# Kernel optimization log

Measured on AMD Instinct MI355X. Metric: run time of the kernel, lower is better.

The kernel has to match this reference:

```python
import jax, jax.numpy as jnp
import numpy as np

N_NODES = 100000
N_EDGES = 3200000
NFEAT = 512
NHID = 256
KEEP_PROB = 0.5  # dropout p = 0.5


def setup_inputs() -> dict:
    key = jax.random.key(0)
    ks = jax.random.split(key, 9)
    x = jax.random.normal(ks[0], (N_NODES, NFEAT), dtype=jnp.float32)
    W1 = jax.random.normal(ks[1], (NFEAT, NHID), dtype=jnp.float32) * (1.0 / np.sqrt(NFEAT))
    b1 = jax.random.normal(ks[2], (NHID,), dtype=jnp.float32) * 0.01
    W2 = jax.random.normal(ks[3], (NHID, NHID), dtype=jnp.float32) * (1.0 / np.sqrt(NHID))
    b2 = jax.random.normal(ks[4], (NHID,), dtype=jnp.float32) * 0.01
    edge_row = jnp.sort(jax.random.randint(ks[5], (N_EDGES,), 0, N_NODES, dtype=jnp.int64))
    edge_col = jax.random.randint(ks[6], (N_EDGES,), 0, N_NODES, dtype=jnp.int64)
    edge_weight = jax.random.uniform(ks[7], (N_EDGES,), dtype=jnp.float32)
    drop_u = jax.random.uniform(ks[8], (N_NODES, NHID), dtype=jnp.float32)
    return {"x": x, "W1": W1, "b1": b1, "W2": W2, "b2": b2,
            "edge_row": edge_row, "edge_col": edge_col,
            "edge_weight": edge_weight, "drop_u": drop_u}


def reference(x, W1, b1, W2, b2, edge_row, edge_col, edge_weight, drop_u):
    n = x.shape[0]

    def spmm(h):
        # out[i] = sum_j adj[i, j] * h[j]  (COO gather + segment-sum)
        msg = h[edge_col] * edge_weight[:, None]  # [E, d]
        return jax.ops.segment_sum(msg, edge_row, num_segments=n)

    # layer 1: relu(spmm(adj, x @ W1) + b1)
    h = jax.nn.relu(spmm(x @ W1) + b1)
    # deterministic dropout (training=True, p=0.5): keep where u < keep_prob, scale by 1/keep
    mask = (drop_u < KEEP_PROB).astype(h.dtype)
    h = h * mask / KEEP_PROB
    # layer 2: relu(spmm(adj, h @ W2) + b2)
    h = jax.nn.relu(spmm(h @ W2) + b2)
    return jax.nn.log_softmax(h, axis=1)
```

## Files before the change

### kernel.cpp

```cpp
#include <hip/hip_runtime.h>
#include <stdint.h>

#define N_NODES 100000
#define N_EDGES 3200000
#define NFEAT 512
#define NHID 256
#define MPAD 100096

typedef __attribute__((ext_vector_type(8))) short bf16x8_t;
typedef __attribute__((ext_vector_type(8))) unsigned short u16x8_t;
typedef __attribute__((ext_vector_type(4))) float f32x4_t;

#define RFL(x) __builtin_amdgcn_readfirstlane(x)

__device__ inline unsigned short f2bf(float f) {
  union { float f; uint32_t u; } x; x.f = f;
  uint32_t r = x.u + 0x7fffu + ((x.u >> 16) & 1u);
  return (unsigned short)(r >> 16);
}
__device__ inline float b2f(unsigned short u) {
  union { uint32_t u; float f; } x; x.u = ((uint32_t)u) << 16;
  return x.f;
}

__global__ void prep_k(const float* __restrict__ W1, const float* __restrict__ W2,
                       unsigned short* __restrict__ W1T, unsigned short* __restrict__ W2T) {
  int i = blockIdx.x * 256 + threadIdx.x;
  if (i < NFEAT * NHID) {
    int k = i >> 8, n = i & 255;
    W1T[n * NFEAT + k] = f2bf(W1[i]);
  } else {
    int j = i - NFEAT * NHID;
    int k = j >> 8, n = j & 255;
    W2T[n * NHID + k] = f2bf(W2[j]);
  }
}

__global__ void rowptr_k(const int* __restrict__ erow, int* __restrict__ rowptr) {
  int r = blockIdx.x * 256 + threadIdx.x;
  if (r > N_NODES) return;
  int lo = 0, hi = N_EDGES;
  while (lo < hi) {
    int mid = (lo + hi) >> 1;
    if (erow[mid] < r) lo = mid + 1; else hi = mid;
  }
  rowptr[r] = lo;
}

template <bool A_FP32>
__global__ __launch_bounds__(512) void gemm_bt2(const void* __restrict__ Ap,
                                                const unsigned short* __restrict__ BT,
                                                unsigned short* __restrict__ C,
                                                int K, int Mreal) {
  __shared__ __align__(16) unsigned short As[128 * 64];
  __shared__ __align__(16) unsigned short Bs[256 * 64];
  const int tid = threadIdx.x;
  const int lane = tid & 63, wid = tid >> 6;
  const int wm = wid >> 2, wn = wid & 3;
  const int m0 = blockIdx.x * 128;
  const int lrow = lane & 15, lhi = lane >> 4;

  f32x4_t acc[4][4] = {};

  const int nt = K >> 6;
  for (int t = 0; t < nt; ++t) {
    __syncthreads();
    if constexpr (A_FP32) {
      const float* A = (const float*)Ap;
      const int rr = tid >> 4;
      const int kq = (tid & 15) << 2;
#pragma unroll
      for (int round = 0; round < 4; ++round) {
        int row = rr + (round << 5);
        int grow = m0 + row; grow = grow < Mreal ? grow : Mreal - 1;
        const f32x4_t v = __builtin_nontemporal_load(
            (const f32x4_t*)(A + (size_t)grow * K + (t << 6) + kq));
        ushort4 b4;
        b4.x = f2bf(v.x); b4.y = f2bf(v.y); b4.z = f2bf(v.z); b4.w = f2bf(v.w);
        *(ushort4*)&As[(row << 6) + (kq ^ ((row & 7) << 3))] = b4;
      }
    } else {
      const unsigned short* A = (const unsigned short*)Ap;
      const int Lrow = tid >> 3;
      const int Lc = (tid & 7) << 4;
#pragma unroll
      for (int round = 0; round < 2; ++round) {
        int row = Lrow + (round << 6);
        int srcc = Lc ^ ((row & 7) << 4);
        const char* g = (const char*)(A + (size_t)(m0 + row) * K + (t << 6)) + srcc;
        __builtin_amdgcn_global_load_lds(
            (const __attribute__((address_space(1))) void*)g,
            (__attribute__((address_space(3))) void*)((char*)As + tid * 16 + (round << 13)),
            16, 0, 0);
      }
    }
    {
      const int Lrow = tid >> 3;
      const int Lc = (tid & 7) << 4;
#pragma unroll
      for (int round = 0; round < 4; ++round) {
        int row = Lrow + (round << 6);
        int srcc = Lc ^ ((row & 7) << 4);
        const char* g = (const char*)(BT + (size_t)row * K + (t << 6)) + srcc;
        __builtin_amdgcn_global_load_lds(
            (const __attribute__((address_space(1))) void*)g,
            (__attribute__((address_space(3))) void*)((char*)Bs + tid * 16 + (round << 13)),
            16, 0, 0);
      }
    }
    asm volatile("s_waitcnt vmcnt(0)" ::: "memory");
    __syncthreads();

#pragma unroll
    for (int ks = 0; ks < 2; ++ks) {
      bf16x8_t af[4], bfr[4];
      const int cu = (ks << 5) + (lhi << 3);
#pragma unroll
      for (int mf = 0; mf < 4; ++mf) {
        int row = (wm << 6) + (mf << 4) + lrow;
        af[mf] = *(const bf16x8_t*)&As[(row << 6) + (cu ^ ((row & 7) << 3))];
      }
#pragma unroll
      for (int nf = 0; nf < 4; ++nf) {
        int row = (wn << 6) + (nf << 4) + lrow;
        bfr[nf] = *(const bf16x8_t*)&Bs[(row << 6) + (cu ^ ((row & 7) << 3))];
      }
#pragma unroll
      for (int mf = 0; mf < 4; ++mf)
#pragma unroll
        for (int nf = 0; nf < 4; ++nf)
          acc[mf][nf] = __builtin_amdgcn_mfma_f32_16x16x32_bf16(af[mf], bfr[nf], acc[mf][nf], 0, 0, 0);
    }
  }

#pragma unroll
  for (int mf = 0; mf < 4; ++mf)
#pragma unroll
    for (int nf = 0; nf < 4; ++nf)
#pragma unroll
      for (int j = 0; j < 4; ++j) {
        int gm = m0 + (wm << 6) + (mf << 4) + (lhi << 2) + j;
        int gn = (wn << 6) + (nf << 4) + lrow;
        C[(size_t)gm * 256 + gn] = f2bf(acc[mf][nf][j]);
      }
}

#define LOADP4(V, W, EB)                                             \
  _Pragma("unroll")                                                  \
  for (int q = 0; q < 4; ++q) {                                      \
    uint32_t ce = (uint32_t)RFL(ecol[(EB) + 2 * q]);                 \
    uint32_t co = (uint32_t)RFL(ecol[(EB) + 2 * q + 1]);             \
    uint32_t ue = RFL(__float_as_uint(ew[(EB) + 2 * q]));            \
    uint32_t uo = RFL(__float_as_uint(ew[(EB) + 2 * q + 1]));        \
    uint32_t cv = lo ? ce : co;                                      \
    W[q] = __uint_as_float(lo ? ue : uo);                            \
    V[q] = *(const u16x8_t*)(Xb + (((size_t)cv << 9) + c16));        \
  }
#define CONSP4(V, W)                                                 \
  _Pragma("unroll")                                                  \
  for (int q = 0; q < 4; ++q)                                        \
    _Pragma("unroll")                                                \
    for (int j = 0; j < 8; ++j)                                      \
      f[j] += W[q] * b2f(V[q][j]);

#define GATHER_ROW()                                                 \
  u16x8_t va[4], vb[4]; float wa[4], wb[4];                          \
  if (e + 8 <= e1) {                                                 \
    LOADP4(va, wa, e);                                               \
    for (; e + 24 <= e1; e += 16) {                                  \
      LOADP4(vb, wb, e + 8);                                         \
      CONSP4(va, wa);                                                \
      LOADP4(va, wa, e + 16);                                        \
      CONSP4(vb, wb);                                                \
    }                                                                \
    if (e + 16 <= e1) {                                              \
      LOADP4(vb, wb, e + 8);                                         \
      CONSP4(va, wa);                                                \
      CONSP4(vb, wb);                                                \
      e += 16;                                                       \
    } else { CONSP4(va, wa); e += 8; }                               \
  }                                                                  \
  for (; e < e1; ++e) {         \
    uint32_t c = (uint32_t)RFL(ecol[e]);                             \
    float w = __uint_as_float(RFL(__float_as_uint(ew[e])));          \
    u16x8_t v = *(const u16x8_t*)(Xb + (((size_t)c << 9) + c16));    \
    float wv = lo ? w : 0.0f;                                        \
    _Pragma("unroll")                                                \
    for (int j = 0; j < 8; ++j) f[j] += wv * b2f(v[j]);              \
  }                                                                  \
  _Pragma("unroll")                                                  \
  for (int j = 0; j < 8; ++j) f[j] += __shfl_xor(f[j], 32);

__global__ __launch_bounds__(256) void spmm1_k(const unsigned short* __restrict__ XW1,
                                               const int* __restrict__ rowptr,
                                               const int* __restrict__ ecol,
                                               const float* __restrict__ ew,
                                               const float* __restrict__ b1,
                                               const float* __restrict__ du,
                                               unsigned short* __restrict__ H) {
  const int lane = threadIdx.x & 63, wid = threadIdx.x >> 6;
  const int r = blockIdx.x * 4 + wid;
  const bool lo = lane < 32;
  const int g = lane & 31;
  const uint32_t c16 = (uint32_t)g << 4;
  if (r >= N_NODES) {
    if (lo) {
      u16x8_t z;
#pragma unroll
      for (int j = 0; j < 8; ++j) z[j] = 0;
      *(u16x8_t*)&H[(size_t)r * 256 + (g << 3)] = z;
    }
    return;
  }
  const char* Xb = (const char*)XW1;
  float f[8] = {};
  int e  = RFL(rowptr[r]);
  const int e1 = RFL(rowptr[r + 1]);
  GATHER_ROW();
  if (lo) {
    const int g8 = g << 3;
    float bv[8], uu[8];
    *(f32x4_t*)&bv[0] = *(const f32x4_t*)&b1[g8];
    *(f32x4_t*)&bv[4] = *(const f32x4_t*)&b1[g8 + 4];
    *(f32x4_t*)&uu[0] = __builtin_nontemporal_load((const f32x4_t*)&du[(size_t)r * 256 + g8]);
    *(f32x4_t*)&uu[4] = __builtin_nontemporal_load((const f32x4_t*)&du[(size_t)r * 256 + g8 + 4]);
    u16x8_t o;
#pragma unroll
    for (int j = 0; j < 8; ++j) {
      float h = fmaxf(f[j] + bv[j], 0.f) * (uu[j] < 0.5f ? 2.f : 0.f);
      o[j] = f2bf(h);
    }
    *(u16x8_t*)&H[(size_t)r * 256 + g8] = o;
  }
}

__global__ __launch_bounds__(256) void spmm2_k(const unsigned short* __restrict__ HW2,
                                               const int* __restrict__ rowptr,
                                               const int* __restrict__ ecol,
                                               const float* __restrict__ ew,
                                               const float* __restrict__ b2,
                                               float* __restrict__ out) {
  const int lane = threadIdx.x & 63, wid = threadIdx.x >> 6;
  const int r = blockIdx.x * 4 + wid;
  if (r >= N_NODES) return;
  const bool lo = lane < 32;
  const int g = lane & 31;
  const uint32_t c16 = (uint32_t)g << 4;
  const char* Xb = (const char*)HW2;
  float f[8] = {};
  int e  = RFL(rowptr[r]);
  const int e1 = RFL(rowptr[r + 1]);
  GATHER_ROW();
  const int g8 = g << 3;
  float bv[8];
  *(f32x4_t*)&bv[0] = *(const f32x4_t*)&b2[g8];
  *(f32x4_t*)&bv[4] = *(const f32x4_t*)&b2[g8 + 4];
  float v[8];
#pragma unroll
  for (int j = 0; j < 8; ++j) v[j] = fmaxf(f[j] + bv[j], 0.f);
  float m = v[0];
#pragma unroll
  for (int j = 1; j < 8; ++j) m = fmaxf(m, v[j]);
#pragma unroll
  for (int off = 16; off > 0; off >>= 1) m = fmaxf(m, __shfl_xor(m, off));
  float s = 0.f;
#pragma unroll
  for (int j = 0; j < 8; ++j) s += expf(v[j] - m);
#pragma unroll
  for (int off = 16; off > 0; off >>= 1) s += __shfl_xor(s, off);
  const float ls = m + logf(s);
  if (lo) {
    f32x4_t o0, o1;
    o0.x = v[0] - ls; o0.y = v[1] - ls; o0.z = v[2] - ls; o0.w = v[3] - ls;
    o1.x = v[4] - ls; o1.y = v[5] - ls; o1.z = v[6] - ls; o1.w = v[7] - ls;
    __builtin_nontemporal_store(o0, (f32x4_t*)&out[(size_t)r * 256 + g8]);
    __builtin_nontemporal_store(o1, (f32x4_t*)&out[(size_t)r * 256 + g8 + 4]);
  }
}

extern "C" void kernel_launch(void* const* d_in, const int* in_sizes, int n_in,
                              void* d_out, int out_size, void* d_ws, size_t ws_size,
                              hipStream_t stream) {
  const float* x  = (const float*)d_in[0];
  const float* W1 = (const float*)d_in[1];
  const float* b1 = (const float*)d_in[2];
  const float* W2 = (const float*)d_in[3];
  const float* b2 = (const float*)d_in[4];
  const int* erow = (const int*)d_in[5];
  const int* ecol = (const int*)d_in[6];
  const float* ew = (const float*)d_in[7];
  const float* du = (const float*)d_in[8];
  float* out = (float*)d_out;

  char* ws = (char*)d_ws;
  unsigned short* W1T = (unsigned short*)ws;
  unsigned short* W2T = (unsigned short*)(ws + 262144);
  int* rowptr = (int*)(ws + 262144 + 131072);
  unsigned short* XW1 = (unsigned short*)(ws + 262144 + 131072 + 401408);
  unsigned short* H = (unsigned short*)(ws + 262144 + 131072 + 401408 + 51249152);

  prep_k<<<768, 256, 0, stream>>>(W1, W2, W1T, W2T);
  rowptr_k<<<392, 256, 0, stream>>>(erow, rowptr);
  gemm_bt2<true><<<782, 512, 0, stream>>>((const void*)x, W1T, XW1, NFEAT, N_NODES);
  spmm1_k<<<MPAD / 4, 256, 0, stream>>>(XW1, rowptr, ecol, ew, b1, du, H);
  gemm_bt2<false><<<782, 512, 0, stream>>>((const void*)H, W2T, XW1, NHID, MPAD);
  spmm2_k<<<N_NODES / 4, 256, 0, stream>>>(XW1, rowptr, ecol, ew, b2, out);
}
```

Measured before the change: 547.6 us.

## Split SpMM gathers into two column-half passes to shrink gather working set

Measured after the change: 547.9 us. Within noise of the previous version (+0.0%).

```diff
diff --git a/kernel.cpp b/kernel.cpp
--- a/kernel.cpp
+++ b/kernel.cpp
@@ -8,7 +8,7 @@
 #define MPAD 100096
 
 typedef __attribute__((ext_vector_type(8))) short bf16x8_t;
-typedef __attribute__((ext_vector_type(8))) unsigned short u16x8_t;
+typedef __attribute__((ext_vector_type(4))) unsigned short u16x4_t;
 typedef __attribute__((ext_vector_type(4))) float f32x4_t;
 
 #define RFL(x) __builtin_amdgcn_readfirstlane(x)
@@ -154,17 +154,17 @@
     uint32_t uo = RFL(__float_as_uint(ew[(EB) + 2 * q + 1]));        \
     uint32_t cv = lo ? ce : co;                                      \
     W[q] = __uint_as_float(lo ? ue : uo);                            \
-    V[q] = *(const u16x8_t*)(Xb + (((size_t)cv << 9) + c16));        \
+    V[q] = *(const u16x4_t*)(Xb + (((size_t)cv << 9) + c8));         \
   }
 #define CONSP4(V, W)                                                 \
   _Pragma("unroll")                                                  \
   for (int q = 0; q < 4; ++q)                                        \
     _Pragma("unroll")                                                \
-    for (int j = 0; j < 8; ++j)                                      \
+    for (int j = 0; j < 4; ++j)                                      \
       f[j] += W[q] * b2f(V[q][j]);
 
 #define GATHER_ROW()                                                 \
-  u16x8_t va[4], vb[4]; float wa[4], wb[4];                          \
+  u16x4_t va[4], vb[4]; float wa[4], wb[4];                          \
   if (e + 8 <= e1) {                                                 \
     LOADP4(va, wa, e);                                               \
     for (; e + 24 <= e1; e += 16) {                                  \
@@ -181,17 +181,18 @@
     } else { CONSP4(va, wa); e += 8; }                               \
   }                                                                  \
   for (; e < e1; ++e) {         \
-    uint32_t c = (uint32_t)RFL(ecol[e]);                             \
-    float w = __uint_as_float(RFL(__float_as_uint(ew[e])));          \
-    u16x8_t v = *(const u16x8_t*)(Xb + (((size_t)c << 9) + c16));    \
-    float wv = lo ? w : 0.0f;                                        \
+    uint32_t c_ = (uint32_t)RFL(ecol[e]);                            \
+    float w_ = __uint_as_float(RFL(__float_as_uint(ew[e])));         \
+    u16x4_t v_ = *(const u16x4_t*)(Xb + (((size_t)c_ << 9) + c8));   \
+    float wv_ = lo ? w_ : 0.0f;                                      \
     _Pragma("unroll")                                                \
-    for (int j = 0; j < 8; ++j) f[j] += wv * b2f(v[j]);              \
+    for (int j = 0; j < 4; ++j) f[j] += wv_ * b2f(v_[j]);            \
   }                                                                  \
   _Pragma("unroll")                                                  \
-  for (int j = 0; j < 8; ++j) f[j] += __shfl_xor(f[j], 32);
-
-__global__ __launch_bounds__(256) void spmm1_k(const unsigned short* __restrict__ XW1,
+  for (int j = 0; j < 4; ++j) f[j] += __shfl_xor(f[j], 32);
+
+template <int P>
+__global__ __launch_bounds__(256) void spmm1_h(const unsigned short* __restrict__ XW1,
                                                const int* __restrict__ rowptr,
                                                const int* __restrict__ ecol,
                                                const float* __restrict__ ew,
@@ -202,80 +203,99 @@
   const int r = blockIdx.x * 4 + wid;
   const bool lo = lane < 32;
   const int g = lane & 31;
-  const uint32_t c16 = (uint32_t)g << 4;
+  const uint32_t c8 = (uint32_t)g << 3;
+  const int g4 = g << 2;
   if (r >= N_NODES) {
     if (lo) {
-      u16x8_t z;
-#pragma unroll
-      for (int j = 0; j < 8; ++j) z[j] = 0;
-      *(u16x8_t*)&H[(size_t)r * 256 + (g << 3)] = z;
+      ushort4 z; z.x = z.y = z.z = z.w = 0;
+      *(ushort4*)&H[(size_t)r * 256 + P * 128 + g4] = z;
     }
     return;
   }
-  const char* Xb = (const char*)XW1;
-  float f[8] = {};
+  const char* Xb = (const char*)XW1 + P * 256;
+  float f[4] = {};
   int e  = RFL(rowptr[r]);
   const int e1 = RFL(rowptr[r + 1]);
   GATHER_ROW();
   if (lo) {
-    const int g8 = g << 3;
-    float bv[8], uu[8];
-    *(f32x4_t*)&bv[0] = *(const f32x4_t*)&b1[g8];
-    *(f32x4_t*)&bv[4] = *(const f32x4_t*)&b1[g8 + 4];
-    *(f32x4_t*)&uu[0] = __builtin_nontemporal_load((const f32x4_t*)&du[(size_t)r * 256 + g8]);
-    *(f32x4_t*)&uu[4] = __builtin_nontemporal_load((const f32x4_t*)&du[(size_t)r * 256 + g8 + 4]);
-    u16x8_t o;
-#pragma unroll
-    for (int j = 0; j < 8; ++j) {
-      float h = fmaxf(f[j] + bv[j], 0.f) * (uu[j] < 0.5f ? 2.f : 0.f);
-      o[j] = f2bf(h);
-    }
-    *(u16x8_t*)&H[(size_t)r * 256 + g8] = o;
-  }
-}
-
-__global__ __launch_bounds__(256) void spmm2_k(const unsigned short* __restrict__ HW2,
-                                               const int* __restrict__ rowptr,
-                                               const int* __restrict__ ecol,
-                                               const float* __restrict__ ew,
-                                               const float* __restrict__ b2,
-                                               float* __restrict__ out) {
+    const int col = P * 128 + g4;
+    const f32x4_t bb = *(const f32x4_t*)&b1[col];
+    const f32x4_t uu = __builtin_nontemporal_load((const f32x4_t*)&du[(size_t)r * 256 + col]);
+    ushort4 o;
+    o.x = f2bf(fmaxf(f[0] + bb.x, 0.f) * (uu.x < 0.5f ? 2.f : 0.f));
+    o.y = f2bf(fmaxf(f[1] + bb.y, 0.f) * (uu.y < 0.5f ? 2.f : 0.f));
+    o.z = f2bf(fmaxf(f[2] + bb.z, 0.f) * (uu.z < 0.5f ? 2.f : 0.f));
+    o.w = f2bf(fmaxf(f[3] + bb.w, 0.f) * (uu.w < 0.5f ? 2.f : 0.f));
+    *(ushort4*)&H[(size_t)r * 256 + col] = o;
+  }
+}
+
+__global__ __launch_bounds__(256) void spmm2_p0(const unsigned short* __restrict__ HW2,
+                                                const int* __restrict__ rowptr,
+                                                const int* __restrict__ ecol,
+                                                const float* __restrict__ ew,
+                                                const float* __restrict__ b2,
+                                                unsigned short* __restrict__ tmp) {
   const int lane = threadIdx.x & 63, wid = threadIdx.x >> 6;
   const int r = blockIdx.x * 4 + wid;
   if (r >= N_NODES) return;
   const bool lo = lane < 32;
   const int g = lane & 31;
-  const uint32_t c16 = (uint32_t)g << 4;
+  const uint32_t c8 = (uint32_t)g << 3;
+  const int g4 = g << 2;
   const char* Xb = (const char*)HW2;
-  float f[8] = {};
+  float f[4] = {};
   int e  = RFL(rowptr[r]);
   const int e1 = RFL(rowptr[r + 1]);
   GATHER_ROW();
-  const int g8 = g << 3;
-  float bv[8];
-  *(f32x4_t*)&bv[0] = *(const f32x4_t*)&b2[g8];
-  *(f32x4_t*)&bv[4] = *(const f32x4_t*)&b2[g8 + 4];
-  float v[8];
-#pragma unroll
-  for (int j = 0; j < 8; ++j) v[j] = fmaxf(f[j] + bv[j], 0.f);
-  float m = v[0];
-#pragma unroll
-  for (int j = 1; j < 8; ++j) m = fmaxf(m, v[j]);
-#pragma unroll
-  for (int off = 16; off > 0; off >>= 1) m = fmaxf(m, __shfl_xor(m, off));
-  float s = 0.f;
-#pragma unroll
-  for (int j = 0; j < 8; ++j) s += expf(v[j] - m);
-#pragma unroll
-  for (int off = 16; off > 0; off >>= 1) s += __shfl_xor(s, off);
+  if (lo) {
+    const f32x4_t bb = *(const f32x4_t*)&b2[g4];
+    ushort4 o;
+    o.x = f2bf(fmaxf(f[0] + bb.x, 0.f));
+    o.y = f2bf(fmaxf(f[1] + bb.y, 0.f));
+    o.z = f2bf(fmaxf(f[2] + bb.z, 0.f));
+    o.w = f2bf(fmaxf(f[3] + bb.w, 0.f));
+    *(ushort4*)&tmp[(size_t)r * 128 + g4] = o;
+  }
+}
+
+__global__ __launch_bounds__(256) void spmm2_p1(const unsigned short* __restrict__ HW2,
+                                                const int* __restrict__ rowptr,
+                                                const int* __restrict__ ecol,
+                                                const float* __restrict__ ew,
+                                                const float* __restrict__ b2,
+                                                const unsigned short* __restrict__ tmp,
+                                                float* __restrict__ out) {
+  const int lane = threadIdx.x & 63, wid = threadIdx.x >> 6;
+  const int r = blockIdx.x * 4 + wid;
+  if (r >= N_NODES) return;
+  const bool lo = lane < 32;
+  const int g = lane & 31;
+  const uint32_t c8 = (uint32_t)g << 3;
+  const int g4 = g << 2;
+  const char* Xb = (const char*)HW2 + 256;
+  float f[4] = {};
+  int e  = RFL(rowptr[r]);
+  const int e1 = RFL(rowptr[r + 1]);
+  GATHER_ROW();
+  const f32x4_t bb = *(const f32x4_t*)&b2[128 + g4];
+  const u16x4_t tv = *(const u16x4_t*)&tmp[(size_t)r * 128 + g4];
+  float val[4];
+  val[0] = lo ? fmaxf(f[0] + bb.x, 0.f) : b2f(tv[0]);
+  val[1] = lo ? fmaxf(f[1] + bb.y, 0.f) : b2f(tv[1]);
+  val[2] = lo ? fmaxf(f[2] + bb.z, 0.f) : b2f(tv[2]);
+  val[3] = lo ? fmaxf(f[3] + bb.w, 0.f) : b2f(tv[3]);
+  float m = fmaxf(fmaxf(val[0], val[1]), fmaxf(val[2], val[3]));
+#pragma unroll
+  for (int off = 32; off > 0; off >>= 1) m = fmaxf(m, __shfl_xor(m, off));
+  float s = expf(val[0] - m) + expf(val[1] - m) + expf(val[2] - m) + expf(val[3] - m);
+#pragma unroll
+  for (int off = 32; off > 0; off >>= 1) s += __shfl_xor(s, off);
   const float ls = m + logf(s);
-  if (lo) {
-    f32x4_t o0, o1;
-    o0.x = v[0] - ls; o0.y = v[1] - ls; o0.z = v[2] - ls; o0.w = v[3] - ls;
-    o1.x = v[4] - ls; o1.y = v[5] - ls; o1.z = v[6] - ls; o1.w = v[7] - ls;
-    __builtin_nontemporal_store(o0, (f32x4_t*)&out[(size_t)r * 256 + g8]);
-    __builtin_nontemporal_store(o1, (f32x4_t*)&out[(size_t)r * 256 + g8 + 4]);
-  }
+  f32x4_t o;
+  o.x = val[0] - ls; o.y = val[1] - ls; o.z = val[2] - ls; o.w = val[3] - ls;
+  const int col = (lo ? 128 : 0) + g4;
+  __builtin_nontemporal_store(o, (f32x4_t*)&out[(size_t)r * 256 + col]);
 }
 
 extern "C" void kernel_launch(void* const* d_in, const int* in_sizes, int n_in,
@@ -298,11 +318,14 @@
   int* rowptr = (int*)(ws + 262144 + 131072);
   unsigned short* XW1 = (unsigned short*)(ws + 262144 + 131072 + 401408);
   unsigned short* H = (unsigned short*)(ws + 262144 + 131072 + 401408 + 51249152);
+  unsigned short* tmp = H;
 
   prep_k<<<768, 256, 0, stream>>>(W1, W2, W1T, W2T);
   rowptr_k<<<392, 256, 0, stream>>>(erow, rowptr);
   gemm_bt2<true><<<782, 512, 0, stream>>>((const void*)x, W1T, XW1, NFEAT, N_NODES);
-  spmm1_k<<<MPAD / 4, 256, 0, stream>>>(XW1, rowptr, ecol, ew, b1, du, H);
+  spmm1_h<0><<<MPAD / 4, 256, 0, stream>>>(XW1, rowptr, ecol, ew, b1, du, H);
+  spmm1_h<1><<<MPAD / 4, 256, 0, stream>>>(XW1, rowptr, ecol, ew, b1, du, H);
   gemm_bt2<false><<<782, 512, 0, stream>>>((const void*)H, W2T, XW1, NHID, MPAD);
-  spmm2_k<<<N_NODES / 4, 256, 0, stream>>>(XW1, rowptr, ecol, ew, b2, out);
-}
+  spmm2_p0<<<N_NODES / 4, 256, 0, stream>>>(XW1, rowptr, ecol, ew, b2, tmp);
+  spmm2_p1<<<N_NODES / 4, 256, 0, stream>>>(XW1, rowptr, ecol, ew, b2, tmp, out);
+}
```
